# Kernel optimization log

Hardware: AMD Instinct MI355X
Metric: run time of the kernel (lower is better)

## Reference

```python
import jax, jax.numpy as jnp
import numpy as np

N_NODES = 50000
N_EDGES = 800000
D = 128
BN_EPS = 1e-5
AGG_EPS = 1e-6


def setup_inputs() -> dict:
    key = jax.random.key(0)
    ks = jax.random.split(key, 20)
    s = 1.0 / np.sqrt(D)
    def w(k):
        return jax.random.normal(k, (D, D), jnp.float32) * s
    def b(k):
        return jax.random.normal(k, (D,), jnp.float32) * 0.01
    return {
        "x": jax.random.normal(ks[0], (N_NODES, D), jnp.float32),
        "e": jax.random.normal(ks[1], (N_EDGES, D), jnp.float32),
        "edge_index": jax.random.randint(ks[2], (2, N_EDGES), 0, N_NODES, jnp.int32),
        "WA": w(ks[3]), "bA": b(ks[4]),
        "WB": w(ks[5]), "bB": b(ks[6]),
        "WC": w(ks[7]), "bC": b(ks[8]),
        "WD": w(ks[9]), "bD": b(ks[10]),
        "WE": w(ks[11]), "bE": b(ks[12]),
        "gamma_x": jnp.ones((D,), jnp.float32), "beta_x": jnp.zeros((D,), jnp.float32),
        "gamma_e": jnp.ones((D,), jnp.float32), "beta_e": jnp.zeros((D,), jnp.float32),
    }


def _batchnorm(v, gamma, beta):
    # training-mode BatchNorm1d: batch stats, biased variance
    mean = v.mean(axis=0)
    var = v.var(axis=0)
    return gamma * (v - mean) * jax.lax.rsqrt(var + BN_EPS) + beta


def reference(x, e, edge_index, WA, bA, WB, bB, WC, bC, WD, bD, WE, bE,
              gamma_x, beta_x, gamma_e, beta_e):
    n_nodes = x.shape[0]
    src = edge_index[0]  # x_j (source)
    dst = edge_index[1]  # x_i (target), aggregation index

    Ax = x @ WA + bA
    Bx = x @ WB + bB
    Ce = e @ WC + bC
    Dx = x @ WD + bD
    Ex = x @ WE + bE

    # message: gather endpoints, gate
    e_ij = Dx[dst] + Ex[src] + Ce            # [n_edges, D]
    sigma_ij = jax.nn.sigmoid(e_ij)

    # aggregate: scatter-sum numerator & denominator, normalize
    num = jax.ops.segment_sum(sigma_ij * Bx[src], dst, num_segments=n_nodes)
    den = jax.ops.segment_sum(sigma_ij, dst, num_segments=n_nodes)
    aggr = num / (den + AGG_EPS)

    # update + BN + ReLU (dropout=0, residual=False per GraphGym wrapper)
    x_out = jax.nn.relu(_batchnorm(Ax + aggr, gamma_x, beta_x))
    e_out = jax.nn.relu(_batchnorm(e_ij, gamma_e, beta_e))
    return x_out, e_out
```

## Files before the change

### kernel.cpp

```cpp
#include <hip/hip_runtime.h>
#include <stdint.h>

#define DD 128
#define NB_G 2048
#define GE   2048

using f32x4  = __attribute__((ext_vector_type(4))) float;
using bf16x8 = __attribute__((ext_vector_type(8))) short;

__device__ __forceinline__ float bf2f(short u) {
  union { unsigned int i; float f; } c;
  c.i = ((unsigned int)(unsigned short)u) << 16;
  return c.f;
}
__device__ __forceinline__ short f2bf(float f) {
  union { float f; unsigned int i; } c;
  c.f = f;
  unsigned int u = c.i;
  u += 0x7fffu + ((u >> 16) & 1u);
  return (short)(u >> 16);
}

__global__ __launch_bounds__(256) void k_zero(int* __restrict__ p, int n) {
  int i = blockIdx.x * 256 + threadIdx.x;
  if (i < n) p[i] = 0;
}

__global__ __launch_bounds__(256) void k_hist(const int* __restrict__ dst, int* __restrict__ deg, int E) {
  int e = blockIdx.x * 256 + threadIdx.x;
  if (e < E) atomicAdd(&deg[dst[e]], 1);
}

__global__ __launch_bounds__(256) void k_scan1(const int* __restrict__ deg, int* __restrict__ off,
                                               int* __restrict__ totals, int n) {
  __shared__ int sm[256];
  int t = threadIdx.x;
  int i = blockIdx.x * 256 + t;
  int v = (i < n) ? deg[i] : 0;
  sm[t] = v;
  __syncthreads();
  int acc = v;
  #pragma unroll
  for (int d = 1; d < 256; d <<= 1) {
    int add = (t >= d) ? sm[t - d] : 0;
    __syncthreads();
    acc += add;
    sm[t] = acc;
    __syncthreads();
  }
  if (i < n) off[i] = acc - v;
  if (t == 255) totals[blockIdx.x] = acc;
}

__global__ __launch_bounds__(256) void k_scan2(const int* __restrict__ totals, int* __restrict__ boff, int nb) {
  __shared__ int sm[256];
  int t = threadIdx.x;
  int v = (t < nb) ? totals[t] : 0;
  sm[t] = v;
  __syncthreads();
  int acc = v;
  #pragma unroll
  for (int d = 1; d < 256; d <<= 1) {
    int add = (t >= d) ? sm[t - d] : 0;
    __syncthreads();
    acc += add;
    sm[t] = acc;
    __syncthreads();
  }
  boff[t] = acc - v;
}

__global__ __launch_bounds__(256) void k_scan3(int* __restrict__ off, const int* __restrict__ boff,
                                               int* __restrict__ cursor, int n) {
  int i = blockIdx.x * 256 + threadIdx.x;
  if (i < n) {
    int o = off[i] + boff[blockIdx.x];
    off[i] = o;
    cursor[i] = o;
  }
}

__global__ __launch_bounds__(256) void k_fill(const int* __restrict__ dst, const int* __restrict__ src,
                                              int* __restrict__ cursor, int* __restrict__ list,
                                              int* __restrict__ srcS, int* __restrict__ posOf, int E) {
  int e = blockIdx.x * 256 + threadIdx.x;
  if (e < E) {
    int p = atomicAdd(&cursor[dst[e]], 1);
    list[p] = e;
    srcS[p] = src[e];
    posOf[e] = p;
  }
}

__global__ __launch_bounds__(256) void k_prewt5(
    const float* __restrict__ WA, const float* __restrict__ WB, const float* __restrict__ WC,
    const float* __restrict__ WD, const float* __restrict__ WE,
    short* __restrict__ WtA, short* __restrict__ WtB, short* __restrict__ WtC,
    short* __restrict__ WtD, short* __restrict__ WtE) {
  const float* Ws[5] = {WA, WB, WC, WD, WE};
  short* Os[5] = {WtA, WtB, WtC, WtD, WtE};
  const float* W = Ws[blockIdx.x];
  short* O = Os[blockIdx.x];
  int t = threadIdx.x, c = t & 127, h = t >> 7;
  for (int p = 0; p < 8; ++p) {
    int k0 = (h * 8 + p) * 8;
    bf16x8 v;
    #pragma unroll
    for (int j = 0; j < 8; ++j) v[j] = f2bf(W[(size_t)(k0 + j) * DD + c]);
    *(bf16x8*)&O[(size_t)c * DD + k0] = v;
  }
}

__global__ __launch_bounds__(256) void k_nodegemm(
    const float* __restrict__ x,
    const short* __restrict__ WtA, const float* __restrict__ bA,
    const short* __restrict__ WtB, const float* __restrict__ bB,
    const short* __restrict__ WtD, const float* __restrict__ bD,
    const short* __restrict__ WtE, const float* __restrict__ bE,
    short* __restrict__ Axh, short* __restrict__ Bxh,
    short* __restrict__ Dxh, short* __restrict__ Exh, int n) {
  int t = threadIdx.x;
  int w = t >> 6, l = t & 63, lg = l >> 4, lc = l & 15;
  int m0 = blockIdx.x * 64;
  int row = m0 + w * 16 + lc;
  bool valid = row < n;
  int rowc = valid ? row : n - 1;

  const float* xr = x + (size_t)rowc * DD;
  bf16x8 af[4];
  #pragma unroll
  for (int kk = 0; kk < 4; ++kk) {
    float4 a0 = *(const float4*)&xr[kk * 32 + lg * 8];
    float4 a1 = *(const float4*)&xr[kk * 32 + lg * 8 + 4];
    af[kk][0] = f2bf(a0.x); af[kk][1] = f2bf(a0.y); af[kk][2] = f2bf(a0.z); af[kk][3] = f2bf(a0.w);
    af[kk][4] = f2bf(a1.x); af[kk][5] = f2bf(a1.y); af[kk][6] = f2bf(a1.z); af[kk][7] = f2bf(a1.w);
  }

  const short* Wt[4] = {WtA, WtB, WtD, WtE};
  const float* bs[4] = {bA, bB, bD, bE};
  short* Os[4] = {Axh, Bxh, Dxh, Exh};

  #pragma unroll
  for (int mi = 0; mi < 4; ++mi) {
    const short* Wm = Wt[mi];
    f32x4 acc[8] = {};
    #pragma unroll
    for (int kk = 0; kk < 4; ++kk) {
      #pragma unroll
      for (int tt = 0; tt < 8; ++tt) {
        bf16x8 bfv = *(const bf16x8*)&Wm[(size_t)(tt * 16 + lc) * DD + kk * 32 + lg * 8];
        acc[tt] = __builtin_amdgcn_mfma_f32_16x16x32_bf16(bfv, af[kk], acc[tt], 0, 0, 0);
      }
    }
    if (valid) {
      short* O = Os[mi];
      #pragma unroll
      for (int tt = 0; tt < 8; ++tt) {
        int f0 = tt * 16 + lg * 4;
        float4 bc = *(const float4*)&bs[mi][f0];
        short4 o;
        o.x = f2bf(acc[tt][0] + bc.x);
        o.y = f2bf(acc[tt][1] + bc.y);
        o.z = f2bf(acc[tt][2] + bc.z);
        o.w = f2bf(acc[tt][3] + bc.w);
        *(short4*)&O[(size_t)row * DD + f0] = o;
      }
    }
  }
}

__global__ __launch_bounds__(256) void k_edge(
    const float* __restrict__ e, const short* __restrict__ WtC, const float* __restrict__ bC,
    const int* __restrict__ srcI, const int* __restrict__ dstI, const int* __restrict__ posOf,
    const short* __restrict__ Dxh, const short* __restrict__ Exh,
    short* __restrict__ eijS, float* __restrict__ pE, int Etot, int ntiles) {
  __shared__ __align__(16) short es[4][16][136];
  __shared__ float sE[4][128], qE[4][128];
  int t = threadIdx.x;
  int w = t >> 6, l = t & 63, lg = l >> 4, lc = l & 15;

  float bCv[8];
  #pragma unroll
  for (int tt = 0; tt < 8; ++tt) bCv[tt] = bC[tt * 16 + lc];

  float se[8] = {}, qe[8] = {};

  const int stride = gridDim.x;
  int tile = blockIdx.x;

  float4 e32[8];
  int dnN[4], snN[4], posN[4];

  {
    size_t m0 = (size_t)tile * 64;
    size_t row = m0 + w * 16 + lc;
    if (row >= (size_t)Etot) row = Etot - 1;
    const float* er = e + row * DD;
    #pragma unroll
    for (int kk = 0; kk < 4; ++kk) {
      e32[kk * 2]     = *(const float4*)&er[kk * 32 + lg * 8];
      e32[kk * 2 + 1] = *(const float4*)&er[kk * 32 + lg * 8 + 4];
    }
    #pragma unroll
    for (int z = 0; z < 4; ++z) {
      size_t erow = m0 + w * 16 + z * 4 + lg;
      if (erow >= (size_t)Etot) erow = Etot - 1;
      dnN[z] = dstI[erow]; snN[z] = srcI[erow]; posN[z] = posOf[erow];
    }
  }

  for (; tile < ntiles; tile += stride) {
    int dn[4], sn[4], pos[4];
    #pragma unroll
    for (int z = 0; z < 4; ++z) { dn[z] = dnN[z]; sn[z] = snN[z]; pos[z] = posN[z]; }

    bf16x8 dv[4], sv[4];
    #pragma unroll
    for (int z = 0; z < 4; ++z) {
      dv[z] = *(const bf16x8*)&Dxh[(size_t)dn[z] * DD + lc * 8];
      sv[z] = *(const bf16x8*)&Exh[(size_t)sn[z] * DD + lc * 8];
    }

    bf16x8 af[4];
    #pragma unroll
    for (int kk = 0; kk < 4; ++kk) {
      float4 a0 = e32[kk * 2], a1 = e32[kk * 2 + 1];
      af[kk][0] = f2bf(a0.x); af[kk][1] = f2bf(a0.y); af[kk][2] = f2bf(a0.z); af[kk][3] = f2bf(a0.w);
      af[kk][4] = f2bf(a1.x); af[kk][5] = f2bf(a1.y); af[kk][6] = f2bf(a1.z); af[kk][7] = f2bf(a1.w);
    }

    int nt = tile + stride;
    if (nt < ntiles) {
      size_t m0n = (size_t)nt * 64;
      size_t row = m0n + w * 16 + lc;
      if (row >= (size_t)Etot) row = Etot - 1;
      const float* er = e + row * DD;
      #pragma unroll
      for (int kk = 0; kk < 4; ++kk) {
        e32[kk * 2]     = *(const float4*)&er[kk * 32 + lg * 8];
        e32[kk * 2 + 1] = *(const float4*)&er[kk * 32 + lg * 8 + 4];
      }
      #pragma unroll
      for (int z = 0; z < 4; ++z) {
        size_t erow = m0n + w * 16 + z * 4 + lg;
        if (erow >= (size_t)Etot) erow = Etot - 1;
        dnN[z] = dstI[erow]; snN[z] = srcI[erow]; posN[z] = posOf[erow];
      }
    }

    f32x4 acc[8] = {};
    #pragma unroll
    for (int kk = 0; kk < 4; ++kk) {
      #pragma unroll
      for (int tt = 0; tt < 8; ++tt) {
        bf16x8 bfv = *(const bf16x8*)&WtC[(size_t)(tt * 16 + lc) * DD + kk * 32 + lg * 8];
        acc[tt] = __builtin_amdgcn_mfma_f32_16x16x32_bf16(af[kk], bfv, acc[tt], 0, 0, 0);
      }
    }

    #pragma unroll
    for (int tt = 0; tt < 8; ++tt) {
      int col = tt * 16 + lc;
      #pragma unroll
      for (int j = 0; j < 4; ++j)
        es[w][lg * 4 + j][col] = f2bf(acc[tt][j] + bCv[tt]);
    }
    asm volatile("s_waitcnt lgkmcnt(0)" ::: "memory");
    __builtin_amdgcn_sched_barrier(0);

    size_t m0 = (size_t)tile * 64;
    #pragma unroll
    for (int z = 0; z < 4; ++z) {
      size_t erow = m0 + w * 16 + z * 4 + lg;
      if (erow < (size_t)Etot) {
        int r = z * 4 + lg;
        bf16x8 cv = *(const bf16x8*)&es[w][r][lc * 8];
        bf16x8 o;
        #pragma unroll
        for (int j = 0; j < 8; ++j) {
          float v = bf2f(cv[j]) + bf2f(dv[z][j]) + bf2f(sv[z][j]);
          se[j] += v; qe[j] += v * v;
          o[j] = f2bf(v);
        }
        *(bf16x8*)&eijS[(size_t)pos[z] * DD + lc * 8] = o;
      }
    }
    __builtin_amdgcn_sched_barrier(0);
  }

  #pragma unroll
  for (int j = 0; j < 8; ++j) {
    se[j] += __shfl_xor(se[j], 16); se[j] += __shfl_xor(se[j], 32);
    qe[j] += __shfl_xor(qe[j], 16); qe[j] += __shfl_xor(qe[j], 32);
  }
  if (lg == 0) {
    #pragma unroll
    for (int j = 0; j < 8; ++j) { sE[w][lc * 8 + j] = se[j]; qE[w][lc * 8 + j] = qe[j]; }
  }
  __syncthreads();
  if (t < 128) {
    float a = sE[0][t] + sE[1][t] + sE[2][t] + sE[3][t];
    float b = qE[0][t] + qE[1][t] + qE[2][t] + qE[3][t];
    pE[(size_t)blockIdx.x * 256 + t] = a;
    pE[(size_t)blockIdx.x * 256 + 128 + t] = b;
  }
}

__global__ __launch_bounds__(256) void k_gather(
    const int* __restrict__ off, const int* __restrict__ deg, const int* __restrict__ list,
    const int* __restrict__ srcS, const short* __restrict__ eijS, const short* __restrict__ Bxh,
    const short* __restrict__ Axh, const float* __restrict__ stE,
    float* __restrict__ outx, float* __restrict__ oute,
    float* __restrict__ pX, int n) {
  int t = threadIdx.x;
  int w = t >> 6, l = t & 63;
  int qw = l >> 4, fi = l & 15;
  int waveId = blockIdx.x * 4 + w;
  const int nwaves = NB_G * 4;

  float su[8], hu[8];
  {
    float4 s0 = *(const float4*)&stE[fi * 8], s1 = *(const float4*)&stE[fi * 8 + 4];
    float4 h0 = *(const float4*)&stE[128 + fi * 8], h1 = *(const float4*)&stE[128 + fi * 8 + 4];
    su[0] = s0.x; su[1] = s0.y; su[2] = s0.z; su[3] = s0.w;
    su[4] = s1.x; su[5] = s1.y; su[6] = s1.z; su[7] = s1.w;
    hu[0] = h0.x; hu[1] = h0.y; hu[2] = h0.z; hu[3] = h0.w;
    hu[4] = h1.x; hu[5] = h1.y; hu[6] = h1.z; hu[7] = h1.w;
  }

  float sx[4] = {}, qx[4] = {};

  for (int node = waveId; node < n; node += nwaves) {
    int start = off[node], dg = deg[node];
    float num[8] = {}, den[8] = {};
    int k = qw;
    for (; k + 4 < dg; k += 8) {
      int p0 = start + k, p1 = start + k + 4;
      int id0 = list[p0], id1 = list[p1];
      int s0 = srcS[p0], s1 = srcS[p1];
      bf16x8 e0 = *(const bf16x8*)&eijS[(size_t)p0 * DD + fi * 8];
      bf16x8 e1 = *(const bf16x8*)&eijS[(size_t)p1 * DD + fi * 8];
      bf16x8 b0 = *(const bf16x8*)&Bxh[(size_t)s0 * DD + fi * 8];
      bf16x8 b1 = *(const bf16x8*)&Bxh[(size_t)s1 * DD + fi * 8];
      float4 oa, ob, oc, od;
      float v0a[8], v1a[8];
      #pragma unroll
      for (int j = 0; j < 8; ++j) {
        float v0 = bf2f(e0[j]), v1 = bf2f(e1[j]);
        v0a[j] = fmaxf(0.f, v0 * su[j] + hu[j]);
        v1a[j] = fmaxf(0.f, v1 * su[j] + hu[j]);
        float g0 = 1.f / (1.f + __expf(-v0)), g1 = 1.f / (1.f + __expf(-v1));
        num[j] += g0 * bf2f(b0[j]) + g1 * bf2f(b1[j]);
        den[j] += g0 + g1;
      }
      oa.x = v0a[0]; oa.y = v0a[1]; oa.z = v0a[2]; oa.w = v0a[3];
      ob.x = v0a[4]; ob.y = v0a[5]; ob.z = v0a[6]; ob.w = v0a[7];
      oc.x = v1a[0]; oc.y = v1a[1]; oc.z = v1a[2]; oc.w = v1a[3];
      od.x = v1a[4]; od.y = v1a[5]; od.z = v1a[6]; od.w = v1a[7];
      *(float4*)&oute[(size_t)id0 * DD + fi * 8] = oa;
      *(float4*)&oute[(size_t)id0 * DD + fi * 8 + 4] = ob;
      *(float4*)&oute[(size_t)id1 * DD + fi * 8] = oc;
      *(float4*)&oute[(size_t)id1 * DD + fi * 8 + 4] = od;
    }
    for (; k < dg; k += 4) {
      int p0 = start + k;
      int id0 = list[p0];
      int s0 = srcS[p0];
      bf16x8 e0 = *(const bf16x8*)&eijS[(size_t)p0 * DD + fi * 8];
      bf16x8 b0 = *(const bf16x8*)&Bxh[(size_t)s0 * DD + fi * 8];
      float4 oa, ob;
      float v0a[8];
      #pragma unroll
      for (int j = 0; j < 8; ++j) {
        float v0 = bf2f(e0[j]);
        v0a[j] = fmaxf(0.f, v0 * su[j] + hu[j]);
        float g0 = 1.f / (1.f + __expf(-v0));
        num[j] += g0 * bf2f(b0[j]);
        den[j] += g0;
      }
      oa.x = v0a[0]; oa.y = v0a[1]; oa.z = v0a[2]; oa.w = v0a[3];
      ob.x = v0a[4]; ob.y = v0a[5]; ob.z = v0a[6]; ob.w = v0a[7];
      *(float4*)&oute[(size_t)id0 * DD + fi * 8] = oa;
      *(float4*)&oute[(size_t)id0 * DD + fi * 8 + 4] = ob;
    }
    #pragma unroll
    for (int j = 0; j < 8; ++j) {
      num[j] += __shfl_xor(num[j], 16); num[j] += __shfl_xor(num[j], 32);
      den[j] += __shfl_xor(den[j], 16); den[j] += __shfl_xor(den[j], 32);
    }
    if (qw < 2) {
      int c0 = fi * 8 + qw * 4;
      short4 ax = *(const short4*)&Axh[(size_t)node * DD + c0];
      short axa[4] = {ax.x, ax.y, ax.z, ax.w};
      float4 o;
      float vv[4];
      #pragma unroll
      for (int j = 0; j < 4; ++j) {
        int jj = qw * 4 + j;
        float aggr = num[jj] / (den[jj] + 1e-6f);
        float xp = bf2f(axa[j]) + aggr;
        vv[j] = xp;
        sx[j] += xp; qx[j] += xp * xp;
      }
      o.x = vv[0]; o.y = vv[1]; o.z = vv[2]; o.w = vv[3];
      *(float4*)&outx[(size_t)node * DD + c0] = o;
    }
  }

  __shared__ float lsX[4][128], lqX[4][128];
  if (qw < 2) {
    #pragma unroll
    for (int j = 0; j < 4; ++j) { lsX[w][fi * 8 + qw * 4 + j] = sx[j]; lqX[w][fi * 8 + qw * 4 + j] = qx[j]; }
  }
  __syncthreads();
  if (t < 128) {
    float a = lsX[0][t] + lsX[1][t] + lsX[2][t] + lsX[3][t];
    float b = lqX[0][t] + lqX[1][t] + lqX[2][t] + lqX[3][t];
    pX[(size_t)blockIdx.x * 256 + t] = a;
    pX[(size_t)blockIdx.x * 256 + 128 + t] = b;
  }
}

__global__ __launch_bounds__(256) void k_reduce(const float* __restrict__ part, int nblk, float invcnt,
                                                const float* __restrict__ gamma, const float* __restrict__ beta,
                                                float* __restrict__ stats) {
  int c = blockIdx.x, t = threadIdx.x;
  float a = 0.f, b = 0.f;
  for (int k = t; k < nblk; k += 256) {
    a += part[(size_t)k * 256 + c];
    b += part[(size_t)k * 256 + 128 + c];
  }
  #pragma unroll
  for (int o = 32; o > 0; o >>= 1) { a += __shfl_down(a, o); b += __shfl_down(b, o); }
  __shared__ float ra[4], rb[4];
  int l = t & 63, w = t >> 6;
  if (l == 0) { ra[w] = a; rb[w] = b; }
  __syncthreads();
  if (t == 0) {
    a = ra[0] + ra[1] + ra[2] + ra[3];
    b = rb[0] + rb[1] + rb[2] + rb[3];
    float mean = a * invcnt;
    float var = b * invcnt - mean * mean;
    float istd = rsqrtf(var + 1e-5f);
    float scale = gamma[c] * istd;
    stats[c] = scale;
    stats[128 + c] = beta[c] - mean * scale;
  }
}

__global__ __launch_bounds__(256) void k_xfinal(float* __restrict__ v, const float* __restrict__ st, size_t n4) {
  size_t i = (size_t)blockIdx.x * 256 + threadIdx.x;
  if (i >= n4) return;
  float4 d = *(const float4*)&v[i * 4];
  int f0 = (int)((i * 4) & 127);
  d.x = fmaxf(0.f, d.x * st[f0 + 0] + st[128 + f0 + 0]);
  d.y = fmaxf(0.f, d.y * st[f0 + 1] + st[128 + f0 + 1]);
  d.z = fmaxf(0.f, d.z * st[f0 + 2] + st[128 + f0 + 2]);
  d.w = fmaxf(0.f, d.w * st[f0 + 3] + st[128 + f0 + 3]);
  *(float4*)&v[i * 4] = d;
}

extern "C" void kernel_launch(void* const* d_in, const int* in_sizes, int n_in,
                              void* d_out, int out_size, void* d_ws, size_t ws_size,
                              hipStream_t stream) {
  const float* x  = (const float*)d_in[0];
  const float* e  = (const float*)d_in[1];
  const int*   ei = (const int*)d_in[2];
  const float* WA = (const float*)d_in[3];  const float* bA = (const float*)d_in[4];
  const float* WB = (const float*)d_in[5];  const float* bB = (const float*)d_in[6];
  const float* WC = (const float*)d_in[7];  const float* bC = (const float*)d_in[8];
  const float* WD = (const float*)d_in[9];  const float* bD = (const float*)d_in[10];
  const float* WE = (const float*)d_in[11]; const float* bE = (const float*)d_in[12];
  const float* gx = (const float*)d_in[13]; const float* bx = (const float*)d_in[14];
  const float* ge = (const float*)d_in[15]; const float* be = (const float*)d_in[16];

  int N = in_sizes[0] / DD;
  int E = in_sizes[2] / 2;
  const int* srcI = ei;
  const int* dstI = ei + E;

  float* outx = (float*)d_out;
  float* oute = (float*)d_out + (size_t)N * DD;

  int ntilesE = (E + 63) / 64;

  char* wp = (char*)d_ws;
  auto alloc = [&](size_t sz) { char* p = wp; wp += (sz + 255) & ~(size_t)255; return p; };
  short* Axh    = (short*)alloc((size_t)N * DD * 2);
  short* Bxh    = (short*)alloc((size_t)N * DD * 2);
  short* Dxh    = (short*)alloc((size_t)N * DD * 2);
  short* Exh    = (short*)alloc((size_t)N * DD * 2);
  short* eijS   = (short*)alloc((size_t)E * DD * 2);
  int*   deg    = (int*)alloc((size_t)N * 4);
  int*   off    = (int*)alloc((size_t)N * 4);
  int*   cursor = (int*)alloc((size_t)N * 4);
  int*   totals = (int*)alloc(1024);
  int*   boff   = (int*)alloc(1024);
  int*   list   = (int*)alloc((size_t)E * 4);
  int*   srcS   = (int*)alloc((size_t)E * 4);
  int*   posOf  = (int*)alloc((size_t)E * 4);
  float* pE     = (float*)alloc((size_t)GE * 256 * 4);
  float* pX     = (float*)alloc((size_t)NB_G * 256 * 4);
  float* statsE = (float*)alloc(1024);
  float* statsX = (float*)alloc(1024);
  short* WtA    = (short*)alloc((size_t)DD * DD * 2);
  short* WtB    = (short*)alloc((size_t)DD * DD * 2);
  short* WtC    = (short*)alloc((size_t)DD * DD * 2);
  short* WtD    = (short*)alloc((size_t)DD * DD * 2);
  short* WtE    = (short*)alloc((size_t)DD * DD * 2);
  (void)ws_size; (void)n_in; (void)out_size;

  int nsb = (N + 255) / 256;

  k_zero<<<nsb, 256, 0, stream>>>(deg, N);
  k_prewt5<<<5, 256, 0, stream>>>(WA, WB, WC, WD, WE, WtA, WtB, WtC, WtD, WtE);
  k_hist<<<(E + 255) / 256, 256, 0, stream>>>(dstI, deg, E);
  k_scan1<<<nsb, 256, 0, stream>>>(deg, off, totals, N);
  k_scan2<<<1, 256, 0, stream>>>(totals, boff, nsb);
  k_scan3<<<nsb, 256, 0, stream>>>(off, boff, cursor, N);
  k_fill<<<(E + 255) / 256, 256, 0, stream>>>(dstI, srcI, cursor, list, srcS, posOf, E);

  k_nodegemm<<<(N + 63) / 64, 256, 0, stream>>>(x, WtA, bA, WtB, bB, WtD, bD, WtE, bE,
                                                Axh, Bxh, Dxh, Exh, N);
  k_edge<<<GE, 256, 0, stream>>>(e, WtC, bC, srcI, dstI, posOf, Dxh, Exh, eijS, pE, E, ntilesE);
  k_reduce<<<128, 256, 0, stream>>>(pE, GE, 1.0f / (float)E, ge, be, statsE);

  k_gather<<<NB_G, 256, 0, stream>>>(off, deg, list, srcS, eijS, Bxh, Axh, statsE,
                                     outx, oute, pX, N);
  k_reduce<<<128, 256, 0, stream>>>(pX, NB_G, 1.0f / (float)N, gx, bx, statsX);
  k_xfinal<<<(int)(((size_t)N * DD / 4 + 255) / 256), 256, 0, stream>>>(outx, statsX, (size_t)N * DD / 4);
}
```

Before: 599.4 us.

## Stage WC in LDS for edge GEMM, per-wave partial stats, unroll gather by four

```diff
diff --git a/kernel.cpp b/kernel.cpp
--- a/kernel.cpp
+++ b/kernel.cpp
@@ -174,10 +174,19 @@
     const int* __restrict__ srcI, const int* __restrict__ dstI, const int* __restrict__ posOf,
     const short* __restrict__ Dxh, const short* __restrict__ Exh,
     short* __restrict__ eijS, float* __restrict__ pE, int Etot, int ntiles) {
+  __shared__ __align__(16) short lds_wt[32 * 64 * 8];
   __shared__ __align__(16) short es[4][16][136];
-  __shared__ float sE[4][128], qE[4][128];
   int t = threadIdx.x;
   int w = t >> 6, l = t & 63, lg = l >> 4, lc = l & 15;
+
+  #pragma unroll
+  for (int i = 0; i < 8; ++i) {
+    int slot = w * 8 + i;
+    int tt = slot >> 2, kk = slot & 3;
+    bf16x8 v = *(const bf16x8*)&WtC[(size_t)(tt * 16 + lc) * DD + kk * 32 + lg * 8];
+    *(bf16x8*)&lds_wt[(slot * 64 + l) * 8] = v;
+  }
+  __syncthreads();
 
   float bCv[8];
   #pragma unroll
@@ -253,7 +262,7 @@
     for (int kk = 0; kk < 4; ++kk) {
       #pragma unroll
       for (int tt = 0; tt < 8; ++tt) {
-        bf16x8 bfv = *(const bf16x8*)&WtC[(size_t)(tt * 16 + lc) * DD + kk * 32 + lg * 8];
+        bf16x8 bfv = *(const bf16x8*)&lds_wt[((tt * 4 + kk) * 64 + l) * 8];
         acc[tt] = __builtin_amdgcn_mfma_f32_16x16x32_bf16(af[kk], bfv, acc[tt], 0, 0, 0);
       }
     }
@@ -294,16 +303,33 @@
     qe[j] += __shfl_xor(qe[j], 16); qe[j] += __shfl_xor(qe[j], 32);
   }
   if (lg == 0) {
-    #pragma unroll
-    for (int j = 0; j < 8; ++j) { sE[w][lc * 8 + j] = se[j]; qE[w][lc * 8 + j] = qe[j]; }
-  }
-  __syncthreads();
-  if (t < 128) {
-    float a = sE[0][t] + sE[1][t] + sE[2][t] + sE[3][t];
-    float b = qE[0][t] + qE[1][t] + qE[2][t] + qE[3][t];
-    pE[(size_t)blockIdx.x * 256 + t] = a;
-    pE[(size_t)blockIdx.x * 256 + 128 + t] = b;
-  }
+    size_t base = ((size_t)blockIdx.x * 4 + w) * 256;
+    #pragma unroll
+    for (int j = 0; j < 8; ++j) {
+      pE[base + lc * 8 + j] = se[j];
+      pE[base + 128 + lc * 8 + j] = qe[j];
+    }
+  }
+}
+
+__device__ __forceinline__ void proc_edge(int id, bf16x8 ev, bf16x8 bv,
+                                          const float* su, const float* hu,
+                                          float* num, float* den,
+                                          float* __restrict__ oute, int fi) {
+  float va[8];
+  #pragma unroll
+  for (int j = 0; j < 8; ++j) {
+    float v0 = bf2f(ev[j]);
+    va[j] = fmaxf(0.f, v0 * su[j] + hu[j]);
+    float g0 = 1.f / (1.f + __expf(-v0));
+    num[j] += g0 * bf2f(bv[j]);
+    den[j] += g0;
+  }
+  float4 oa, ob;
+  oa.x = va[0]; oa.y = va[1]; oa.z = va[2]; oa.w = va[3];
+  ob.x = va[4]; ob.y = va[5]; ob.z = va[6]; ob.w = va[7];
+  *(float4*)&oute[(size_t)id * DD + fi * 8] = oa;
+  *(float4*)&oute[(size_t)id * DD + fi * 8 + 4] = ob;
 }
 
 __global__ __launch_bounds__(256) void k_gather(
@@ -334,33 +360,22 @@
     int start = off[node], dg = deg[node];
     float num[8] = {}, den[8] = {};
     int k = qw;
-    for (; k + 4 < dg; k += 8) {
-      int p0 = start + k, p1 = start + k + 4;
-      int id0 = list[p0], id1 = list[p1];
-      int s0 = srcS[p0], s1 = srcS[p1];
+    for (; k + 12 < dg; k += 16) {
+      int p0 = start + k, p1 = p0 + 4, p2 = p0 + 8, p3 = p0 + 12;
+      int id0 = list[p0], id1 = list[p1], id2 = list[p2], id3 = list[p3];
+      int s0 = srcS[p0], s1 = srcS[p1], s2 = srcS[p2], s3 = srcS[p3];
       bf16x8 e0 = *(const bf16x8*)&eijS[(size_t)p0 * DD + fi * 8];
       bf16x8 e1 = *(const bf16x8*)&eijS[(size_t)p1 * DD + fi * 8];
+      bf16x8 e2 = *(const bf16x8*)&eijS[(size_t)p2 * DD + fi * 8];
+      bf16x8 e3 = *(const bf16x8*)&eijS[(size_t)p3 * DD + fi * 8];
       bf16x8 b0 = *(const bf16x8*)&Bxh[(size_t)s0 * DD + fi * 8];
       bf16x8 b1 = *(const bf16x8*)&Bxh[(size_t)s1 * DD + fi * 8];
-      float4 oa, ob, oc, od;
-      float v0a[8], v1a[8];
-      #pragma unroll
-      for (int j = 0; j < 8; ++j) {
-        float v0 = bf2f(e0[j]), v1 = bf2f(e1[j]);
-        v0a[j] = fmaxf(0.f, v0 * su[j] + hu[j]);
-        v1a[j] = fmaxf(0.f, v1 * su[j] + hu[j]);
-        float g0 = 1.f / (1.f + __expf(-v0)), g1 = 1.f / (1.f + __expf(-v1));
-        num[j] += g0 * bf2f(b0[j]) + g1 * bf2f(b1[j]);
-        den[j] += g0 + g1;
-      }
-      oa.x = v0a[0]; oa.y = v0a[1]; oa.z = v0a[2]; oa.w = v0a[3];
-      ob.x = v0a[4]; ob.y = v0a[5]; ob.z = v0a[6]; ob.w = v0a[7];
-      oc.x = v1a[0]; oc.y = v1a[1]; oc.z = v1a[2]; oc.w = v1a[3];
-      od.x = v1a[4]; od.y = v1a[5]; od.z = v1a[6]; od.w = v1a[7];
-      *(float4*)&oute[(size_t)id0 * DD + fi * 8] = oa;
-      *(float4*)&oute[(size_t)id0 * DD + fi * 8 + 4] = ob;
-      *(float4*)&oute[(size_t)id1 * DD + fi * 8] = oc;
-      *(float4*)&oute[(size_t)id1 * DD + fi * 8 + 4] = od;
+      bf16x8 b2 = *(const bf16x8*)&Bxh[(size_t)s2 * DD + fi * 8];
+      bf16x8 b3 = *(const bf16x8*)&Bxh[(size_t)s3 * DD + fi * 8];
+      proc_edge(id0, e0, b0, su, hu, num, den, oute, fi);
+      proc_edge(id1, e1, b1, su, hu, num, den, oute, fi);
+      proc_edge(id2, e2, b2, su, hu, num, den, oute, fi);
+      proc_edge(id3, e3, b3, su, hu, num, den, oute, fi);
     }
     for (; k < dg; k += 4) {
       int p0 = start + k;
@@ -368,20 +383,7 @@
       int s0 = srcS[p0];
       bf16x8 e0 = *(const bf16x8*)&eijS[(size_t)p0 * DD + fi * 8];
       bf16x8 b0 = *(const bf16x8*)&Bxh[(size_t)s0 * DD + fi * 8];
-      float4 oa, ob;
-      float v0a[8];
-      #pragma unroll
-      for (int j = 0; j < 8; ++j) {
-        float v0 = bf2f(e0[j]);
-        v0a[j] = fmaxf(0.f, v0 * su[j] + hu[j]);
-        float g0 = 1.f / (1.f + __expf(-v0));
-        num[j] += g0 * bf2f(b0[j]);
-        den[j] += g0;
-      }
-      oa.x = v0a[0]; oa.y = v0a[1]; oa.z = v0a[2]; oa.w = v0a[3];
-      ob.x = v0a[4]; ob.y = v0a[5]; ob.z = v0a[6]; ob.w = v0a[7];
-      *(float4*)&oute[(size_t)id0 * DD + fi * 8] = oa;
-      *(float4*)&oute[(size_t)id0 * DD + fi * 8 + 4] = ob;
+      proc_edge(id0, e0, b0, su, hu, num, den, oute, fi);
     }
     #pragma unroll
     for (int j = 0; j < 8; ++j) {
@@ -499,7 +501,7 @@
   int*   list   = (int*)alloc((size_t)E * 4);
   int*   srcS   = (int*)alloc((size_t)E * 4);
   int*   posOf  = (int*)alloc((size_t)E * 4);
-  float* pE     = (float*)alloc((size_t)GE * 256 * 4);
+  float* pE     = (float*)alloc((size_t)GE * 4 * 256 * 4);
   float* pX     = (float*)alloc((size_t)NB_G * 256 * 4);
   float* statsE = (float*)alloc(1024);
   float* statsX = (float*)alloc(1024);
@@ -523,7 +525,7 @@
   k_nodegemm<<<(N + 63) / 64, 256, 0, stream>>>(x, WtA, bA, WtB, bB, WtD, bD, WtE, bE,
                                                 Axh, Bxh, Dxh, Exh, N);
   k_edge<<<GE, 256, 0, stream>>>(e, WtC, bC, srcI, dstI, posOf, Dxh, Exh, eijS, pE, E, ntilesE);
-  k_reduce<<<128, 256, 0, stream>>>(pE, GE, 1.0f / (float)E, ge, be, statsE);
+  k_reduce<<<128, 256, 0, stream>>>(pE, GE * 4, 1.0f / (float)E, ge, be, statsE);
 
   k_gather<<<NB_G, 256, 0, stream>>>(off, deg, list, srcS, eijS, Bxh, Axh, statsE,
                                      outx, oute, pX, N);
```

Result: faster. 580.5 us (-3.2%).
